# Optimization experiments

Hardware: AMD Instinct MI355X
Metric: run time of the kernel (lower is better)

## Reference

```python
import jax, jax.numpy as jnp
import numpy as np

N_NODES = 50000
LN_EPS = 1e-5


def setup_inputs() -> dict:
    key = jax.random.key(0)
    ks = jax.random.split(key, 8)
    d = 128
    E = 800000
    x = jax.random.normal(ks[0], (N_NODES, d), dtype=jnp.float32)
    edge_index = jax.random.randint(ks[1], (2, E), 0, N_NODES, dtype=jnp.int64)
    edge_weight = jax.random.uniform(ks[2], (E,), dtype=jnp.float32)
    s = 1.0 / np.sqrt(d)
    W1 = jax.random.normal(ks[3], (d, d), dtype=jnp.float32) * s
    W2 = jax.random.normal(ks[4], (d, d), dtype=jnp.float32) * s
    return {
        'x': x, 'edge_index': edge_index, 'edge_weight': edge_weight,
        'W1': W1, 'b1': jnp.zeros((d,), jnp.float32),
        'W2': W2, 'b2': jnp.zeros((d,), jnp.float32),
        'g1': jnp.ones((d,), jnp.float32), 'be1': jnp.zeros((d,), jnp.float32),
        'g2': jnp.ones((d,), jnp.float32), 'be2': jnp.zeros((d,), jnp.float32),
    }


def _layer_norm(h, gamma, beta):
    mu = jnp.mean(h, axis=-1, keepdims=True)
    var = jnp.mean(jnp.square(h - mu), axis=-1, keepdims=True)
    return (h - mu) * jax.lax.rsqrt(var + LN_EPS) * gamma + beta


def _gcn_layer(h, W, b, src, dst, ew):
    # GCNConv(add_self_loops=False, normalize=False): linear then edge scatter-add
    h = h @ W                                    # [N, d]
    msg = h[src] * ew[:, None]                   # [E, d] gather + weight
    agg = jax.ops.segment_sum(msg, dst, num_segments=N_NODES)  # scatter-add at target
    return agg + b


def reference(x, edge_index, edge_weight, W1, b1, W2, b2, g1, be1, g2, be2):
    src, dst = edge_index[0], edge_index[1]  # PyG: messages flow source -> target
    h = _gcn_layer(x, W1, b1, src, dst, edge_weight)
    h = jax.nn.relu(_layer_norm(h, g1, be1))  # dropout = identity (eval)
    h = _gcn_layer(h, W2, b2, src, dst, edge_weight)
    h = jax.nn.relu(_layer_norm(h, g2, be2))
    return h
```

## Files before the change

### kernel.cpp

```cpp
#include <hip/hip_runtime.h>
#include <hip/hip_fp16.h>
#include <stdint.h>

#define LN_EPS 1e-5f
#define G1 256
#define P1CAP 4096
#define P3CAP 6144
#define CAPB 6144

typedef __attribute__((ext_vector_type(8))) short s16x8;
typedef __attribute__((ext_vector_type(4))) float f32x4;

__device__ __forceinline__ float b2f(unsigned short u) {
    union { unsigned int i; float f; } v; v.i = ((unsigned int)u) << 16; return v.f;
}
__device__ __forceinline__ unsigned short f2b(float f) {
    union { float f; unsigned int i; } v; v.f = f;
    unsigned int u = v.i;
    return (unsigned short)((u + 0x7fffu + ((u >> 16) & 1u)) >> 16);
}
__device__ __forceinline__ unsigned int pk2(float a, float b) {
    return (unsigned int)f2b(a) | ((unsigned int)f2b(b) << 16);
}
__device__ __forceinline__ __half2 u2h2(unsigned int u) {
    union { unsigned int i; __half2 h; } v; v.i = u; return v.h;
}

__device__ __forceinline__ float rdf(const void* p, int i, int f32flag) {
    return f32flag ? ((const float*)p)[i] : b2f(((const unsigned short*)p)[i]);
}

__global__ void k_prep(const void* W1, const void* W2,
                       const void* b1, const void* b2,
                       const void* g1, const void* g2,
                       const void* be1, const void* be2,
                       unsigned short* __restrict__ Wt1, unsigned short* __restrict__ Wt2,
                       float* __restrict__ sm, const int* __restrict__ flags) {
    int t = threadIdx.x;
    int f = flags[0];
    int i = blockIdx.x * 256 + t;
    int k = i >> 7, j = i & 127;
    Wt1[j * 128 + k] = f2b(rdf(W1, i, f));
    Wt2[j * 128 + k] = f2b(rdf(W2, i, f));
    if (blockIdx.x == 0 && t < 128) {
        sm[t]       = rdf(b1, t, f);
        sm[128 + t] = rdf(b2, t, f);
        sm[256 + t] = rdf(g1, t, f);
        sm[384 + t] = rdf(g2, t, f);
        sm[512 + t] = rdf(be1, t, f);
        sm[640 + t] = rdf(be2, t, f);
    }
}

__global__ __launch_bounds__(256) void k_p1(const unsigned short* __restrict__ xu,
                                            const int* __restrict__ ei, const void* __restrict__ ew,
                                            int E, int B, int chunk,
                                            unsigned int* __restrict__ gA,
                                            unsigned char* __restrict__ g8,
                                            int* __restrict__ cnt2d, int* __restrict__ lofs2d,
                                            int* __restrict__ flags) {
    __shared__ int hist[256], cur[256], tmp[256];
    __shared__ unsigned int bin32[P1CAP];
    __shared__ unsigned char bin8[P1CAP];
    int t = threadIdx.x, g = blockIdx.x;
    if (t < 2) hist[t] = 0;
    __syncthreads();
    int c1 = 0;
    for (int i = t; i < 2048; i += 256)
        if (fabsf(b2f(xu[i])) > 1e6f) ++c1;
    if (c1) atomicAdd(&hist[0], c1);
    int mn = (E < 1024) ? E : 1024;
    int z = 0;
    for (int i = t; i < mn; i += 256)
        if (ei[2 * i + 1] == 0) ++z;
    if (z) atomicAdd(&hist[1], z);
    __syncthreads();
    int f32f = (hist[0] > 32) ? 1 : 0;
    int f64  = (hist[1] > (mn >> 1)) ? 1 : 0;
    if (g == 0 && t == 0) { flags[0] = f32f; flags[1] = f64; }
    __syncthreads();
    int base = g * chunk;
    int cnt = E - base; if (cnt > chunk) cnt = chunk; if (cnt < 0) cnt = 0;
    hist[t] = 0;
    __syncthreads();
    for (int i = t; i < cnt; i += 256) {
        int e = base + i;
        int d = f64 ? ei[2 * E + 2 * e] : ei[E + e];
        atomicAdd(&hist[d >> 8], 1);
    }
    __syncthreads();
    int v = hist[t];
    tmp[t] = v;
    __syncthreads();
    for (int d = 1; d < 256; d <<= 1) {
        int x = (t >= d) ? tmp[t - d] : 0;
        __syncthreads();
        tmp[t] += x;
        __syncthreads();
    }
    int excl = tmp[t] - v;
    cur[t] = excl;
    if (t < B) { cnt2d[t * G1 + g] = v; lofs2d[t * G1 + g] = excl; }
    __syncthreads();
    for (int i = t; i < cnt; i += 256) {
        int e = base + i;
        int d, sN;
        if (f64) { d = ei[2 * E + 2 * e]; sN = ei[2 * e]; }
        else     { d = ei[E + e];         sN = ei[e]; }
        float w = f32f ? ((const float*)ew)[e] : b2f(((const unsigned short*)ew)[e]);
        __half wh = __float2half(w);
        int p = atomicAdd(&cur[d >> 8], 1);
        bin32[p] = (unsigned int)(sN & 0xffff) | ((unsigned int)__half_as_ushort(wh) << 16);
        bin8[p]  = (unsigned char)(d & 255);
    }
    __syncthreads();
    for (int j = t; j < cnt; j += 256) {
        gA[base + j] = bin32[j];
        g8[base + j] = bin8[j];
    }
}

__global__ __launch_bounds__(256) void k_p3(const unsigned int* __restrict__ gA,
                                            const unsigned char* __restrict__ g8,
                                            const int* __restrict__ cnt2d,
                                            const int* __restrict__ lofs2d,
                                            unsigned int* __restrict__ edata,
                                            uint2* __restrict__ nfo,
                                            int N, int B, int chunk) {
    __shared__ unsigned int raw[P3CAP];
    __shared__ unsigned int srt[CAPB];
    __shared__ unsigned char r8[P3CAP];
    __shared__ int h[256], tmp[256];
    __shared__ int s_cnt;
    int b = blockIdx.x, t = threadIdx.x;
    int segc = cnt2d[b * G1 + t];
    int sbase = t * chunk + lofs2d[b * G1 + t];
    int v = segc;
    tmp[t] = v;
    __syncthreads();
    for (int d = 1; d < 256; d <<= 1) {
        int x = (t >= d) ? tmp[t - d] : 0;
        __syncthreads();
        tmp[t] += x;
        __syncthreads();
    }
    int lo = tmp[t] - v;
    if (t == 255) s_cnt = tmp[255];
    int j = 0;
    for (; j + 3 < segc; j += 4) {
        unsigned int a0 = gA[sbase + j], a1 = gA[sbase + j + 1];
        unsigned int a2 = gA[sbase + j + 2], a3 = gA[sbase + j + 3];
        unsigned char c0 = g8[sbase + j], c1 = g8[sbase + j + 1];
        unsigned char c2 = g8[sbase + j + 2], c3 = g8[sbase + j + 3];
        int i0 = lo + j;
        if (i0 + 3 < P3CAP) {
            raw[i0] = a0; raw[i0 + 1] = a1; raw[i0 + 2] = a2; raw[i0 + 3] = a3;
            r8[i0] = c0; r8[i0 + 1] = c1; r8[i0 + 2] = c2; r8[i0 + 3] = c3;
        }
    }
    for (; j < segc; ++j) {
        int idx = lo + j;
        if (idx < P3CAP) { raw[idx] = gA[sbase + j]; r8[idx] = g8[sbase + j]; }
    }
    h[t] = 0;
    __syncthreads();
    int cnt = s_cnt; if (cnt > P3CAP) cnt = P3CAP;
    for (int i = t; i < cnt; i += 256) atomicAdd(&h[r8[i]], 1);
    __syncthreads();
    int deg = h[t];
    int pd = (deg + 7) & ~7;
    tmp[t] = pd;
    __syncthreads();
    for (int d = 1; d < 256; d <<= 1) {
        int x = (t >= d) ? tmp[t - d] : 0;
        __syncthreads();
        tmp[t] += x;
        __syncthreads();
    }
    int pexcl = tmp[t] - pd;
    int padTot = tmp[255]; if (padTot > CAPB) padTot = CAPB;
    int node0 = b << 8;
    int gbase = b * CAPB;
    if (node0 + t < N) nfo[node0 + t] = make_uint2((unsigned)(gbase + pexcl), (unsigned)deg);
    h[t] = pexcl;
    for (int i = t; i < padTot; i += 256) srt[i] = 0;
    __syncthreads();
    for (int i = t; i < cnt; i += 256) {
        int p = atomicAdd(&h[r8[i]], 1);
        if (p < CAPB) srt[p] = raw[i];
    }
    __syncthreads();
    for (int i = t; i < padTot; i += 256) edata[gbase + i] = srt[i];
}

__global__ __launch_bounds__(256) void k_gemm(const void* __restrict__ X,
                                              const unsigned short* __restrict__ Wt,
                                              unsigned short* __restrict__ Hh, int N,
                                              const int* __restrict__ flags, int layer1) {
    __shared__ unsigned char lds[49152];
    unsigned char* xs = lds;
    unsigned char* wt = lds + 16384;
    int t = threadIdx.x;
    int node0 = blockIdx.x * 64;
    int f32in = layer1 ? flags[0] : 0;

#pragma unroll
    for (int it = 0; it < 8; ++it) {
        int c = t + it * 256;
        int row = c >> 4, cc = c & 15;
        uint4 v = *(const uint4*)(Wt + row * 128 + cc * 8);
        int off = (row * 256 + cc * 16) ^ ((row & 7) << 4);
        *(uint4*)(wt + off) = v;
    }
#pragma unroll
    for (int it = 0; it < 4; ++it) {
        int c = t + it * 256;
        int row = c >> 4, cc = c & 15;
        int g = node0 + row;
        uint4 v = make_uint4(0, 0, 0, 0);
        if (g < N) {
            if (f32in) {
                const float* xr = (const float*)X + (size_t)g * 128 + cc * 8;
                float4 f0 = *(const float4*)xr;
                float4 f1 = *(const float4*)(xr + 4);
                v.x = pk2(f0.x, f0.y); v.y = pk2(f0.z, f0.w);
                v.z = pk2(f1.x, f1.y); v.w = pk2(f1.z, f1.w);
            } else {
                v = *(const uint4*)((const unsigned short*)X + (size_t)g * 128 + cc * 8);
            }
        }
        int off = (row * 256 + cc * 16) ^ ((row & 7) << 4);
        *(uint4*)(xs + off) = v;
    }
    __syncthreads();

    int w = t >> 6, l = t & 63;
    int arow = l & 15;
    int apart = l >> 4;
    f32x4 acc[8];
#pragma unroll
    for (int ct = 0; ct < 8; ++ct) acc[ct] = (f32x4){0.f, 0.f, 0.f, 0.f};

#pragma unroll
    for (int ks = 0; ks < 4; ++ks) {
        int grow = w * 16 + arow;
        int aoff = (grow * 256 + ks * 64 + apart * 16) ^ ((grow & 7) << 4);
        s16x8 afrag = *(const s16x8*)(xs + aoff);
#pragma unroll
        for (int ct = 0; ct < 8; ++ct) {
            int brow = ct * 16 + arow;
            int boff = (brow * 256 + ks * 64 + apart * 16) ^ ((brow & 7) << 4);
            s16x8 bfrag = *(const s16x8*)(wt + boff);
            acc[ct] = __builtin_amdgcn_mfma_f32_16x16x32_bf16(afrag, bfrag, acc[ct], 0, 0, 0);
        }
    }
    int orow0 = node0 + w * 16 + apart * 4;
    int ocol = arow;
#pragma unroll
    for (int ct = 0; ct < 8; ++ct) {
#pragma unroll
        for (int r = 0; r < 4; ++r) {
            int g = orow0 + r;
            if (g < N) {
                __half hh = __float2half(acc[ct][r]);
                Hh[(size_t)g * 128 + ct * 16 + ocol] = __half_as_ushort(hh);
            }
        }
    }
}

template <bool FINAL>
__global__ __launch_bounds__(256) void k_agg_ln(const unsigned short* __restrict__ Hh,
                                                const unsigned int* __restrict__ edata,
                                                const uint2* __restrict__ nfo,
                                                const float* __restrict__ bias,
                                                const float* __restrict__ g,
                                                const float* __restrict__ be,
                                                unsigned short* __restrict__ outb,
                                                void* __restrict__ outAny,
                                                const int* __restrict__ flags, int N) {
    int t = threadIdx.x;
    int l16 = t & 15;
    int node = blockIdx.x * 16 + (t >> 4);
    if (node >= N) return;
    uint2 info = nfo[node];
    int base = (int)info.x, deg = (int)info.y;
    __half2 a01 = u2h2(0u), a23 = u2h2(0u), a45 = u2h2(0u), a67 = u2h2(0u);
    const uint4* Hl = (const uint4*)Hh + l16;
    for (int b0 = 0; b0 < deg; b0 += 8) {
        const uint4* ep = (const uint4*)(edata + base + b0);
        uint4 q0 = ep[0], q1 = ep[1];
        uint4 h0 = Hl[(size_t)(q0.x & 0xffffu) << 4];
        uint4 h1 = Hl[(size_t)(q0.y & 0xffffu) << 4];
        uint4 h2 = Hl[(size_t)(q0.z & 0xffffu) << 4];
        uint4 h3 = Hl[(size_t)(q0.w & 0xffffu) << 4];
        uint4 h4 = Hl[(size_t)(q1.x & 0xffffu) << 4];
        uint4 h5 = Hl[(size_t)(q1.y & 0xffffu) << 4];
        uint4 h6 = Hl[(size_t)(q1.z & 0xffffu) << 4];
        uint4 h7 = Hl[(size_t)(q1.w & 0xffffu) << 4];
        unsigned int wb; __half2 w2;
#define ACC8(hh, wsrc)                                                        \
        wb = (wsrc) >> 16; w2 = u2h2(wb | (wb << 16));                        \
        a01 = __hfma2(u2h2(hh.x), w2, a01); a23 = __hfma2(u2h2(hh.y), w2, a23); \
        a45 = __hfma2(u2h2(hh.z), w2, a45); a67 = __hfma2(u2h2(hh.w), w2, a67);
        ACC8(h0, q0.x) ACC8(h1, q0.y) ACC8(h2, q0.z) ACC8(h3, q0.w)
        ACC8(h4, q1.x) ACC8(h5, q1.y) ACC8(h6, q1.z) ACC8(h7, q1.w)
#undef ACC8
    }
    float4 bv0 = ((const float4*)bias)[2 * l16];
    float4 bv1 = ((const float4*)bias)[2 * l16 + 1];
    float a0 = __low2float(a01) + bv0.x, a1 = __high2float(a01) + bv0.y;
    float a2 = __low2float(a23) + bv0.z, a3 = __high2float(a23) + bv0.w;
    float a4 = __low2float(a45) + bv1.x, a5 = __high2float(a45) + bv1.y;
    float a6 = __low2float(a67) + bv1.z, a7 = __high2float(a67) + bv1.w;
    float s = ((a0 + a1) + (a2 + a3)) + ((a4 + a5) + (a6 + a7));
#pragma unroll
    for (int m = 8; m >= 1; m >>= 1) s += __shfl_xor(s, m, 64);
    float mu = s * (1.f / 128.f);
    float d0 = a0 - mu, d1 = a1 - mu, d2 = a2 - mu, d3 = a3 - mu;
    float d4 = a4 - mu, d5 = a5 - mu, d6 = a6 - mu, d7 = a7 - mu;
    float q = ((d0 * d0 + d1 * d1) + (d2 * d2 + d3 * d3)) +
              ((d4 * d4 + d5 * d5) + (d6 * d6 + d7 * d7));
#pragma unroll
    for (int m = 8; m >= 1; m >>= 1) q += __shfl_xor(q, m, 64);
    float rs = rsqrtf(q * (1.f / 128.f) + LN_EPS);
    float4 gv0 = ((const float4*)g)[2 * l16], gv1 = ((const float4*)g)[2 * l16 + 1];
    float4 bev0 = ((const float4*)be)[2 * l16], bev1 = ((const float4*)be)[2 * l16 + 1];
    float r0 = fmaxf(d0 * rs * gv0.x + bev0.x, 0.f);
    float r1 = fmaxf(d1 * rs * gv0.y + bev0.y, 0.f);
    float r2 = fmaxf(d2 * rs * gv0.z + bev0.z, 0.f);
    float r3 = fmaxf(d3 * rs * gv0.w + bev0.w, 0.f);
    float r4 = fmaxf(d4 * rs * gv1.x + bev1.x, 0.f);
    float r5 = fmaxf(d5 * rs * gv1.y + bev1.y, 0.f);
    float r6 = fmaxf(d6 * rs * gv1.z + bev1.z, 0.f);
    float r7 = fmaxf(d7 * rs * gv1.w + bev1.w, 0.f);
    if (FINAL) {
        if (flags[0]) {
            float4* o = (float4*)outAny + (size_t)node * 32 + 2 * l16;
            o[0] = make_float4(r0, r1, r2, r3);
            o[1] = make_float4(r4, r5, r6, r7);
        } else {
            uint4 o;
            o.x = pk2(r0, r1); o.y = pk2(r2, r3);
            o.z = pk2(r4, r5); o.w = pk2(r6, r7);
            ((uint4*)outAny)[(size_t)node * 16 + l16] = o;
        }
    } else {
        uint4 o;
        o.x = pk2(r0, r1); o.y = pk2(r2, r3);
        o.z = pk2(r4, r5); o.w = pk2(r6, r7);
        ((uint4*)outb)[(size_t)node * 16 + l16] = o;
    }
}

extern "C" void kernel_launch(void* const* d_in, const int* in_sizes, int n_in,
                              void* d_out, int out_size, void* d_ws, size_t ws_size,
                              hipStream_t stream) {
    const unsigned short* x_u16 = (const unsigned short*)d_in[0];
    const int*            ei    = (const int*)d_in[1];

    const int N = in_sizes[0] / 128;
    const int E = in_sizes[2];
    const int B = (N + 255) >> 8;
    const int chunk = (E + G1 - 1) / G1;

    unsigned short* Xb = (unsigned short*)d_ws;
    unsigned short* Hh = Xb + (size_t)N * 128;
    unsigned int* gA    = (unsigned int*)(Hh + (size_t)N * 128);
    unsigned int* edata = gA + E;
    unsigned char* g8   = (unsigned char*)(edata + (size_t)B * CAPB);
    int* cnt2d  = (int*)(g8 + ((E + 3) & ~3));
    int* lofs2d = cnt2d + 65536;
    uint2* nfo  = (uint2*)(lofs2d + 65536);
    int* flags  = (int*)(nfo + N);
    unsigned short* Wt1 = (unsigned short*)(flags + 8);
    unsigned short* Wt2 = Wt1 + 16384;
    float* sm   = (float*)(Wt2 + 16384);
    float* b1f  = sm;
    float* b2f_ = sm + 128;
    float* g1f  = sm + 256;
    float* g2f  = sm + 384;
    float* be1f = sm + 512;
    float* be2f = sm + 640;

    const int nodeBlocks = (N + 15) / 16;
    const int gemmBlocks = (N + 63) / 64;

    k_p1<<<G1, 256, 0, stream>>>(x_u16, ei, d_in[2], E, B, chunk, gA, g8, cnt2d, lofs2d, flags);
    k_prep<<<64, 256, 0, stream>>>(d_in[3], d_in[5], d_in[4], d_in[6],
                                   d_in[7], d_in[9], d_in[8], d_in[10],
                                   Wt1, Wt2, sm, flags);
    k_p3<<<B, 256, 0, stream>>>(gA, g8, cnt2d, lofs2d, edata, nfo, N, B, chunk);

    k_gemm<<<gemmBlocks, 256, 0, stream>>>(d_in[0], Wt1, Hh, N, flags, 1);
    k_agg_ln<false><<<nodeBlocks, 256, 0, stream>>>(Hh, edata, nfo, b1f, g1f, be1f, Xb, nullptr, flags, N);

    k_gemm<<<gemmBlocks, 256, 0, stream>>>(Xb, Wt2, Hh, N, flags, 0);
    k_agg_ln<true><<<nodeBlocks, 256, 0, stream>>>(Hh, edata, nfo, b2f_, g2f, be2f, nullptr, d_out, flags, N);
}
```

Baseline: 121.7 us.

## Merge weight prep into partition kernel, degree-sort nodes, prefetch edge indices

Folds the weight-transpose/param-conversion kernel into extra blocks of the first partition kernel, removing one launch. Within each 256-node bucket, nodes are reordered by degree via a counting sort, so the 16 nodes sharing a wavefront/block have similar degrees and less loop divergence; the original node id is packed into the high bits of the degree field. The aggregation loop also software-prefetches the next 8 edge entries before processing the current ones. This adds a second histogram/scan in the bucketing kernel and limits degree and local index to 16 bits.

```diff
diff --git a/kernel.cpp b/kernel.cpp
--- a/kernel.cpp
+++ b/kernel.cpp
@@ -30,30 +30,15 @@
     return f32flag ? ((const float*)p)[i] : b2f(((const unsigned short*)p)[i]);
 }
 
-__global__ void k_prep(const void* W1, const void* W2,
-                       const void* b1, const void* b2,
-                       const void* g1, const void* g2,
-                       const void* be1, const void* be2,
-                       unsigned short* __restrict__ Wt1, unsigned short* __restrict__ Wt2,
-                       float* __restrict__ sm, const int* __restrict__ flags) {
-    int t = threadIdx.x;
-    int f = flags[0];
-    int i = blockIdx.x * 256 + t;
-    int k = i >> 7, j = i & 127;
-    Wt1[j * 128 + k] = f2b(rdf(W1, i, f));
-    Wt2[j * 128 + k] = f2b(rdf(W2, i, f));
-    if (blockIdx.x == 0 && t < 128) {
-        sm[t]       = rdf(b1, t, f);
-        sm[128 + t] = rdf(b2, t, f);
-        sm[256 + t] = rdf(g1, t, f);
-        sm[384 + t] = rdf(g2, t, f);
-        sm[512 + t] = rdf(be1, t, f);
-        sm[640 + t] = rdf(be2, t, f);
-    }
-}
-
 __global__ __launch_bounds__(256) void k_p1(const unsigned short* __restrict__ xu,
                                             const int* __restrict__ ei, const void* __restrict__ ew,
+                                            const void* W1, const void* W2,
+                                            const void* b1, const void* b2_,
+                                            const void* g1, const void* g2,
+                                            const void* be1, const void* be2,
+                                            unsigned short* __restrict__ Wt1,
+                                            unsigned short* __restrict__ Wt2,
+                                            float* __restrict__ sm,
                                             int E, int B, int chunk,
                                             unsigned int* __restrict__ gA,
                                             unsigned char* __restrict__ g8,
@@ -78,6 +63,22 @@
     int f32f = (hist[0] > 32) ? 1 : 0;
     int f64  = (hist[1] > (mn >> 1)) ? 1 : 0;
     if (g == 0 && t == 0) { flags[0] = f32f; flags[1] = f64; }
+
+    if (g >= G1) {
+        int i = (g - G1) * 256 + t;
+        int k = i >> 7, j = i & 127;
+        Wt1[j * 128 + k] = f2b(rdf(W1, i, f32f));
+        Wt2[j * 128 + k] = f2b(rdf(W2, i, f32f));
+        if (g == G1 && t < 128) {
+            sm[t]       = rdf(b1, t, f32f);
+            sm[128 + t] = rdf(b2_, t, f32f);
+            sm[256 + t] = rdf(g1, t, f32f);
+            sm[384 + t] = rdf(g2, t, f32f);
+            sm[512 + t] = rdf(be1, t, f32f);
+            sm[640 + t] = rdf(be2, t, f32f);
+        }
+        return;
+    }
     __syncthreads();
     int base = g * chunk;
     int cnt = E - base; if (cnt > chunk) cnt = chunk; if (cnt < 0) cnt = 0;
@@ -180,8 +181,8 @@
     int pexcl = tmp[t] - pd;
     int padTot = tmp[255]; if (padTot > CAPB) padTot = CAPB;
     int node0 = b << 8;
+    int nn = N - node0; if (nn > 256) nn = 256;
     int gbase = b * CAPB;
-    if (node0 + t < N) nfo[node0 + t] = make_uint2((unsigned)(gbase + pexcl), (unsigned)deg);
     h[t] = pexcl;
     for (int i = t; i < padTot; i += 256) srt[i] = 0;
     __syncthreads();
@@ -191,6 +192,29 @@
     }
     __syncthreads();
     for (int i = t; i < padTot; i += 256) edata[gbase + i] = srt[i];
+    h[t] = 0;
+    __syncthreads();
+    int dcl = (deg > 255) ? 255 : deg;
+    if (t < nn) atomicAdd(&h[dcl], 1);
+    __syncthreads();
+    v = h[t];
+    tmp[t] = v;
+    __syncthreads();
+    for (int d = 1; d < 256; d <<= 1) {
+        int x = (t >= d) ? tmp[t - d] : 0;
+        __syncthreads();
+        tmp[t] += x;
+        __syncthreads();
+    }
+    int excl2 = tmp[t] - v;
+    __syncthreads();
+    h[t] = excl2;
+    __syncthreads();
+    if (t < nn) {
+        int rank = atomicAdd(&h[dcl], 1);
+        nfo[node0 + rank] = make_uint2((unsigned)(gbase + pexcl),
+                                       (unsigned)deg | ((unsigned)t << 16));
+    }
 }
 
 __global__ __launch_bounds__(256) void k_gemm(const void* __restrict__ X,
@@ -281,15 +305,21 @@
                                                 const int* __restrict__ flags, int N) {
     int t = threadIdx.x;
     int l16 = t & 15;
-    int node = blockIdx.x * 16 + (t >> 4);
-    if (node >= N) return;
-    uint2 info = nfo[node];
-    int base = (int)info.x, deg = (int)info.y;
+    int idx = blockIdx.x * 16 + (t >> 4);
+    if (idx >= N) return;
+    uint2 info = nfo[idx];
+    int base = (int)info.x;
+    int deg = (int)(info.y & 0xffffu);
+    int node = (idx & ~255) | (int)(info.y >> 16);
     __half2 a01 = u2h2(0u), a23 = u2h2(0u), a45 = u2h2(0u), a67 = u2h2(0u);
     const uint4* Hl = (const uint4*)Hh + l16;
-    for (int b0 = 0; b0 < deg; b0 += 8) {
-        const uint4* ep = (const uint4*)(edata + base + b0);
-        uint4 q0 = ep[0], q1 = ep[1];
+    const uint4* ep = (const uint4*)(edata + base);
+    int nb = (deg + 7) >> 3;
+    uint4 q0 = make_uint4(0, 0, 0, 0), q1 = q0;
+    if (nb > 0) { q0 = ep[0]; q1 = ep[1]; }
+    for (int ib = 0; ib < nb; ++ib) {
+        uint4 p0 = q0, p1 = q1;
+        if (ib + 1 < nb) { p0 = ep[2 * ib + 2]; p1 = ep[2 * ib + 3]; }
         uint4 h0 = Hl[(size_t)(q0.x & 0xffffu) << 4];
         uint4 h1 = Hl[(size_t)(q0.y & 0xffffu) << 4];
         uint4 h2 = Hl[(size_t)(q0.z & 0xffffu) << 4];
@@ -306,6 +336,7 @@
         ACC8(h0, q0.x) ACC8(h1, q0.y) ACC8(h2, q0.z) ACC8(h3, q0.w)
         ACC8(h4, q1.x) ACC8(h5, q1.y) ACC8(h6, q1.z) ACC8(h7, q1.w)
 #undef ACC8
+        q0 = p0; q1 = p1;
     }
     float4 bv0 = ((const float4*)bias)[2 * l16];
     float4 bv1 = ((const float4*)bias)[2 * l16 + 1];
@@ -386,10 +417,11 @@
     const int nodeBlocks = (N + 15) / 16;
     const int gemmBlocks = (N + 63) / 64;
 
-    k_p1<<<G1, 256, 0, stream>>>(x_u16, ei, d_in[2], E, B, chunk, gA, g8, cnt2d, lofs2d, flags);
-    k_prep<<<64, 256, 0, stream>>>(d_in[3], d_in[5], d_in[4], d_in[6],
-                                   d_in[7], d_in[9], d_in[8], d_in[10],
-                                   Wt1, Wt2, sm, flags);
+    k_p1<<<G1 + 64, 256, 0, stream>>>(x_u16, ei, d_in[2],
+                                      d_in[3], d_in[5], d_in[4], d_in[6],
+                                      d_in[7], d_in[9], d_in[8], d_in[10],
+                                      Wt1, Wt2, sm,
+                                      E, B, chunk, gA, g8, cnt2d, lofs2d, flags);
     k_p3<<<B, 256, 0, stream>>>(gA, g8, cnt2d, lofs2d, edata, nfo, N, B, chunk);
 
     k_gemm<<<gemmBlocks, 256, 0, stream>>>(d_in[0], Wt1, Hh, N, flags, 1);
```

Result: slower. 126.4 us (+3.9%).

## Merge weight prep into binning kernel and run bucket sort beside layer-1 GEMM

Applied to the files above, without the earlier changes.

The weight transpose/conversion is folded into k_p1 as extra blocks, and the per-bucket sort (k_p3) is fused with the layer-1 GEMM into one launch where the first B blocks sort and the rest do the GEMM. This removes two kernel launches and lets the sort and the GEMM, which are independent, run at the same time. The sort now writes zero padding and scattered edges straight to global memory instead of staging them in LDS, which adds scattered global writes. The GEMM blocks in the fused kernel must reserve 48KB of LDS, which may lower occupancy for the sort blocks.

```diff
diff --git a/kernel.cpp b/kernel.cpp
--- a/kernel.cpp
+++ b/kernel.cpp
@@ -30,30 +30,15 @@
     return f32flag ? ((const float*)p)[i] : b2f(((const unsigned short*)p)[i]);
 }
 
-__global__ void k_prep(const void* W1, const void* W2,
-                       const void* b1, const void* b2,
-                       const void* g1, const void* g2,
-                       const void* be1, const void* be2,
-                       unsigned short* __restrict__ Wt1, unsigned short* __restrict__ Wt2,
-                       float* __restrict__ sm, const int* __restrict__ flags) {
-    int t = threadIdx.x;
-    int f = flags[0];
-    int i = blockIdx.x * 256 + t;
-    int k = i >> 7, j = i & 127;
-    Wt1[j * 128 + k] = f2b(rdf(W1, i, f));
-    Wt2[j * 128 + k] = f2b(rdf(W2, i, f));
-    if (blockIdx.x == 0 && t < 128) {
-        sm[t]       = rdf(b1, t, f);
-        sm[128 + t] = rdf(b2, t, f);
-        sm[256 + t] = rdf(g1, t, f);
-        sm[384 + t] = rdf(g2, t, f);
-        sm[512 + t] = rdf(be1, t, f);
-        sm[640 + t] = rdf(be2, t, f);
-    }
-}
-
 __global__ __launch_bounds__(256) void k_p1(const unsigned short* __restrict__ xu,
                                             const int* __restrict__ ei, const void* __restrict__ ew,
+                                            const void* W1, const void* W2,
+                                            const void* b1, const void* b2_,
+                                            const void* g1, const void* g2,
+                                            const void* be1, const void* be2,
+                                            unsigned short* __restrict__ Wt1,
+                                            unsigned short* __restrict__ Wt2,
+                                            float* __restrict__ sm,
                                             int E, int B, int chunk,
                                             unsigned int* __restrict__ gA,
                                             unsigned char* __restrict__ g8,
@@ -78,6 +63,22 @@
     int f32f = (hist[0] > 32) ? 1 : 0;
     int f64  = (hist[1] > (mn >> 1)) ? 1 : 0;
     if (g == 0 && t == 0) { flags[0] = f32f; flags[1] = f64; }
+
+    if (g >= G1) {
+        int i = (g - G1) * 256 + t;
+        int k = i >> 7, j = i & 127;
+        Wt1[j * 128 + k] = f2b(rdf(W1, i, f32f));
+        Wt2[j * 128 + k] = f2b(rdf(W2, i, f32f));
+        if (g == G1 && t < 128) {
+            sm[t]       = rdf(b1, t, f32f);
+            sm[128 + t] = rdf(b2_, t, f32f);
+            sm[256 + t] = rdf(g1, t, f32f);
+            sm[384 + t] = rdf(g2, t, f32f);
+            sm[512 + t] = rdf(be1, t, f32f);
+            sm[640 + t] = rdf(be2, t, f32f);
+        }
+        return;
+    }
     __syncthreads();
     int base = g * chunk;
     int cnt = E - base; if (cnt > chunk) cnt = chunk; if (cnt < 0) cnt = 0;
@@ -120,89 +121,90 @@
     }
 }
 
-__global__ __launch_bounds__(256) void k_p3(const unsigned int* __restrict__ gA,
-                                            const unsigned char* __restrict__ g8,
-                                            const int* __restrict__ cnt2d,
-                                            const int* __restrict__ lofs2d,
-                                            unsigned int* __restrict__ edata,
-                                            uint2* __restrict__ nfo,
-                                            int N, int B, int chunk) {
-    __shared__ unsigned int raw[P3CAP];
-    __shared__ unsigned int srt[CAPB];
-    __shared__ unsigned char r8[P3CAP];
-    __shared__ int h[256], tmp[256];
-    __shared__ int s_cnt;
-    int b = blockIdx.x, t = threadIdx.x;
-    int segc = cnt2d[b * G1 + t];
-    int sbase = t * chunk + lofs2d[b * G1 + t];
-    int v = segc;
-    tmp[t] = v;
-    __syncthreads();
-    for (int d = 1; d < 256; d <<= 1) {
-        int x = (t >= d) ? tmp[t - d] : 0;
-        __syncthreads();
-        tmp[t] += x;
-        __syncthreads();
-    }
-    int lo = tmp[t] - v;
-    if (t == 255) s_cnt = tmp[255];
-    int j = 0;
-    for (; j + 3 < segc; j += 4) {
-        unsigned int a0 = gA[sbase + j], a1 = gA[sbase + j + 1];
-        unsigned int a2 = gA[sbase + j + 2], a3 = gA[sbase + j + 3];
-        unsigned char c0 = g8[sbase + j], c1 = g8[sbase + j + 1];
-        unsigned char c2 = g8[sbase + j + 2], c3 = g8[sbase + j + 3];
-        int i0 = lo + j;
-        if (i0 + 3 < P3CAP) {
-            raw[i0] = a0; raw[i0 + 1] = a1; raw[i0 + 2] = a2; raw[i0 + 3] = a3;
-            r8[i0] = c0; r8[i0 + 1] = c1; r8[i0 + 2] = c2; r8[i0 + 3] = c3;
-        }
-    }
-    for (; j < segc; ++j) {
-        int idx = lo + j;
-        if (idx < P3CAP) { raw[idx] = gA[sbase + j]; r8[idx] = g8[sbase + j]; }
-    }
-    h[t] = 0;
-    __syncthreads();
-    int cnt = s_cnt; if (cnt > P3CAP) cnt = P3CAP;
-    for (int i = t; i < cnt; i += 256) atomicAdd(&h[r8[i]], 1);
-    __syncthreads();
-    int deg = h[t];
-    int pd = (deg + 7) & ~7;
-    tmp[t] = pd;
-    __syncthreads();
-    for (int d = 1; d < 256; d <<= 1) {
-        int x = (t >= d) ? tmp[t - d] : 0;
-        __syncthreads();
-        tmp[t] += x;
-        __syncthreads();
-    }
-    int pexcl = tmp[t] - pd;
-    int padTot = tmp[255]; if (padTot > CAPB) padTot = CAPB;
-    int node0 = b << 8;
-    int gbase = b * CAPB;
-    if (node0 + t < N) nfo[node0 + t] = make_uint2((unsigned)(gbase + pexcl), (unsigned)deg);
-    h[t] = pexcl;
-    for (int i = t; i < padTot; i += 256) srt[i] = 0;
-    __syncthreads();
-    for (int i = t; i < cnt; i += 256) {
-        int p = atomicAdd(&h[r8[i]], 1);
-        if (p < CAPB) srt[p] = raw[i];
-    }
-    __syncthreads();
-    for (int i = t; i < padTot; i += 256) edata[gbase + i] = srt[i];
-}
-
-__global__ __launch_bounds__(256) void k_gemm(const void* __restrict__ X,
-                                              const unsigned short* __restrict__ Wt,
-                                              unsigned short* __restrict__ Hh, int N,
-                                              const int* __restrict__ flags, int layer1) {
+__global__ __launch_bounds__(256) void k_p3g(const unsigned int* __restrict__ gA,
+                                             const unsigned char* __restrict__ g8,
+                                             const int* __restrict__ cnt2d,
+                                             const int* __restrict__ lofs2d,
+                                             unsigned int* __restrict__ edata,
+                                             uint2* __restrict__ nfo,
+                                             const void* __restrict__ X,
+                                             const unsigned short* __restrict__ Wt,
+                                             unsigned short* __restrict__ Hh,
+                                             const int* __restrict__ flags,
+                                             int N, int B, int chunk) {
     __shared__ unsigned char lds[49152];
+    int t = threadIdx.x, g = blockIdx.x;
+
+    if (g < B) {
+        unsigned int* raw = (unsigned int*)lds;
+        unsigned char* r8 = lds + 24576;
+        int* h   = (int*)(lds + 30720);
+        int* tmp = (int*)(lds + 31744);
+        int* s_cnt = (int*)(lds + 32768);
+        int b = g;
+        int segc = cnt2d[b * G1 + t];
+        int sbase = t * chunk + lofs2d[b * G1 + t];
+        int v = segc;
+        tmp[t] = v;
+        __syncthreads();
+        for (int d = 1; d < 256; d <<= 1) {
+            int x = (t >= d) ? tmp[t - d] : 0;
+            __syncthreads();
+            tmp[t] += x;
+            __syncthreads();
+        }
+        int lo = tmp[t] - v;
+        if (t == 255) s_cnt[0] = tmp[255];
+        int j = 0;
+        for (; j + 3 < segc; j += 4) {
+            unsigned int a0 = gA[sbase + j], a1 = gA[sbase + j + 1];
+            unsigned int a2 = gA[sbase + j + 2], a3 = gA[sbase + j + 3];
+            unsigned char c0 = g8[sbase + j], c1 = g8[sbase + j + 1];
+            unsigned char c2 = g8[sbase + j + 2], c3 = g8[sbase + j + 3];
+            int i0 = lo + j;
+            if (i0 + 3 < P3CAP) {
+                raw[i0] = a0; raw[i0 + 1] = a1; raw[i0 + 2] = a2; raw[i0 + 3] = a3;
+                r8[i0] = c0; r8[i0 + 1] = c1; r8[i0 + 2] = c2; r8[i0 + 3] = c3;
+            }
+        }
+        for (; j < segc; ++j) {
+            int idx = lo + j;
+            if (idx < P3CAP) { raw[idx] = gA[sbase + j]; r8[idx] = g8[sbase + j]; }
+        }
+        h[t] = 0;
+        __syncthreads();
+        int cnt = s_cnt[0]; if (cnt > P3CAP) cnt = P3CAP;
+        for (int i = t; i < cnt; i += 256) atomicAdd(&h[r8[i]], 1);
+        __syncthreads();
+        int deg = h[t];
+        int pd = (deg + 7) & ~7;
+        tmp[t] = pd;
+        __syncthreads();
+        for (int d = 1; d < 256; d <<= 1) {
+            int x = (t >= d) ? tmp[t - d] : 0;
+            __syncthreads();
+            tmp[t] += x;
+            __syncthreads();
+        }
+        int pexcl = tmp[t] - pd;
+        int padTot = tmp[255]; if (padTot > CAPB) padTot = CAPB;
+        int node0 = b << 8;
+        int gbase = b * CAPB;
+        if (node0 + t < N) nfo[node0 + t] = make_uint2((unsigned)(gbase + pexcl), (unsigned)deg);
+        h[t] = pexcl;
+        for (int i = t; i < padTot; i += 256) edata[gbase + i] = 0;
+        __syncthreads();
+        for (int i = t; i < cnt; i += 256) {
+            int p = atomicAdd(&h[r8[i]], 1);
+            if (p < CAPB) edata[gbase + p] = raw[i];
+        }
+        return;
+    }
+
     unsigned char* xs = lds;
     unsigned char* wt = lds + 16384;
-    int t = threadIdx.x;
-    int node0 = blockIdx.x * 64;
-    int f32in = layer1 ? flags[0] : 0;
+    int node0 = (g - B) * 64;
+    int f32in = flags[0];
 
 #pragma unroll
     for (int it = 0; it < 8; ++it) {
@@ -216,19 +218,83 @@
     for (int it = 0; it < 4; ++it) {
         int c = t + it * 256;
         int row = c >> 4, cc = c & 15;
-        int g = node0 + row;
+        int gg = node0 + row;
         uint4 v = make_uint4(0, 0, 0, 0);
-        if (g < N) {
+        if (gg < N) {
             if (f32in) {
-                const float* xr = (const float*)X + (size_t)g * 128 + cc * 8;
+                const float* xr = (const float*)X + (size_t)gg * 128 + cc * 8;
                 float4 f0 = *(const float4*)xr;
                 float4 f1 = *(const float4*)(xr + 4);
                 v.x = pk2(f0.x, f0.y); v.y = pk2(f0.z, f0.w);
                 v.z = pk2(f1.x, f1.y); v.w = pk2(f1.z, f1.w);
             } else {
-                v = *(const uint4*)((const unsigned short*)X + (size_t)g * 128 + cc * 8);
+                v = *(const uint4*)((const unsigned short*)X + (size_t)gg * 128 + cc * 8);
             }
         }
+        int off = (row * 256 + cc * 16) ^ ((row & 7) << 4);
+        *(uint4*)(xs + off) = v;
+    }
+    __syncthreads();
+
+    int w = t >> 6, l = t & 63;
+    int arow = l & 15;
+    int apart = l >> 4;
+    f32x4 acc[8];
+#pragma unroll
+    for (int ct = 0; ct < 8; ++ct) acc[ct] = (f32x4){0.f, 0.f, 0.f, 0.f};
+
+#pragma unroll
+    for (int ks = 0; ks < 4; ++ks) {
+        int grow = w * 16 + arow;
+        int aoff = (grow * 256 + ks * 64 + apart * 16) ^ ((grow & 7) << 4);
+        s16x8 afrag = *(const s16x8*)(xs + aoff);
+#pragma unroll
+        for (int ct = 0; ct < 8; ++ct) {
+            int brow = ct * 16 + arow;
+            int boff = (brow * 256 + ks * 64 + apart * 16) ^ ((brow & 7) << 4);
+            s16x8 bfrag = *(const s16x8*)(wt + boff);
+            acc[ct] = __builtin_amdgcn_mfma_f32_16x16x32_bf16(afrag, bfrag, acc[ct], 0, 0, 0);
+        }
+    }
+    int orow0 = node0 + w * 16 + apart * 4;
+    int ocol = arow;
+#pragma unroll
+    for (int ct = 0; ct < 8; ++ct) {
+#pragma unroll
+        for (int r = 0; r < 4; ++r) {
+            int gg = orow0 + r;
+            if (gg < N) {
+                __half hh = __float2half(acc[ct][r]);
+                Hh[(size_t)gg * 128 + ct * 16 + ocol] = __half_as_ushort(hh);
+            }
+        }
+    }
+}
+
+__global__ __launch_bounds__(256) void k_gemm(const unsigned short* __restrict__ X,
+                                              const unsigned short* __restrict__ Wt,
+                                              unsigned short* __restrict__ Hh, int N) {
+    __shared__ unsigned char lds[49152];
+    unsigned char* xs = lds;
+    unsigned char* wt = lds + 16384;
+    int t = threadIdx.x;
+    int node0 = blockIdx.x * 64;
+
+#pragma unroll
+    for (int it = 0; it < 8; ++it) {
+        int c = t + it * 256;
+        int row = c >> 4, cc = c & 15;
+        uint4 v = *(const uint4*)(Wt + row * 128 + cc * 8);
+        int off = (row * 256 + cc * 16) ^ ((row & 7) << 4);
+        *(uint4*)(wt + off) = v;
+    }
+#pragma unroll
+    for (int it = 0; it < 4; ++it) {
+        int c = t + it * 256;
+        int row = c >> 4, cc = c & 15;
+        int g = node0 + row;
+        uint4 v = make_uint4(0, 0, 0, 0);
+        if (g < N) v = *(const uint4*)(X + (size_t)g * 128 + cc * 8);
         int off = (row * 256 + cc * 16) ^ ((row & 7) << 4);
         *(uint4*)(xs + off) = v;
     }
@@ -386,15 +452,17 @@
     const int nodeBlocks = (N + 15) / 16;
     const int gemmBlocks = (N + 63) / 64;
 
-    k_p1<<<G1, 256, 0, stream>>>(x_u16, ei, d_in[2], E, B, chunk, gA, g8, cnt2d, lofs2d, flags);
-    k_prep<<<64, 256, 0, stream>>>(d_in[3], d_in[5], d_in[4], d_in[6],
-                                   d_in[7], d_in[9], d_in[8], d_in[10],
-                                   Wt1, Wt2, sm, flags);
-    k_p3<<<B, 256, 0, stream>>>(gA, g8, cnt2d, lofs2d, edata, nfo, N, B, chunk);
-
-    k_gemm<<<gemmBlocks, 256, 0, stream>>>(d_in[0], Wt1, Hh, N, flags, 1);
+    k_p1<<<G1 + 64, 256, 0, stream>>>(x_u16, ei, d_in[2],
+                                      d_in[3], d_in[5], d_in[4], d_in[6],
+                                      d_in[7], d_in[9], d_in[8], d_in[10],
+                                      Wt1, Wt2, sm,
+                                      E, B, chunk, gA, g8, cnt2d, lofs2d, flags);
+
+    k_p3g<<<B + gemmBlocks, 256, 0, stream>>>(gA, g8, cnt2d, lofs2d, edata, nfo,
+                                              d_in[0], Wt1, Hh, flags, N, B, chunk);
+
     k_agg_ln<false><<<nodeBlocks, 256, 0, stream>>>(Hh, edata, nfo, b1f, g1f, be1f, Xb, nullptr, flags, N);
 
-    k_gemm<<<gemmBlocks, 256, 0, stream>>>(Xb, Wt2, Hh, N, flags, 0);
+    k_gemm<<<gemmBlocks, 256, 0, stream>>>(Xb, Wt2, Hh, N);
     k_agg_ln<true><<<nodeBlocks, 256, 0, stream>>>(Hh, edata, nfo, b2f_, g2f, be2f, nullptr, d_out, flags, N);
 }
```

Result: faster. 110.0 us (-9.6%).
